# Kernel tuning notes

Measured on AMD Instinct MI355X. Metric: run time of the kernel, lower is better.

Reference implementation:

```python
import jax, jax.numpy as jnp
import numpy as np

N = 4096
F_IN = 256
HEADS = 8
FEAT = 64
NEG_SLOPE = 0.2


def setup_inputs() -> dict:
    key = jax.random.key(0)
    k_x, k_adj, k_w, k_s, k_d = jax.random.split(key, 5)
    x = jax.random.normal(k_x, (N, F_IN), dtype=jnp.float32)
    adj = (jax.random.uniform(k_adj, (N, N)) < 0.02).astype(jnp.float32)
    W = jax.random.normal(k_w, (F_IN, HEADS * FEAT), dtype=jnp.float32) * (1.0 / np.sqrt(F_IN))
    a_src = jax.random.normal(k_s, (FEAT,), dtype=jnp.float32) * (1.0 / np.sqrt(FEAT))
    a_dst = jax.random.normal(k_d, (FEAT,), dtype=jnp.float32) * (1.0 / np.sqrt(FEAT))
    return {"x": x, "adj": adj, "W": W, "a_src": a_src, "a_dst": a_dst}


def reference(x, adj, W, a_src, a_dst):
    n = x.shape[0]
    adj = adj + jnp.eye(n, dtype=adj.dtype)          # add self loops
    h = (x @ W).reshape(n, HEADS, FEAT)              # (N, H, F)
    s_src = jnp.einsum('nhf,f->nh', h, a_src)        # (N, H)
    s_dst = jnp.einsum('nhf,f->nh', h, a_dst)        # (N, H)
    # e[i, j, h] = leaky_relu(s_src[i,h] + s_dst[j,h])  -> (N, N, H)
    e = jax.nn.leaky_relu(s_src[:, None, :] + s_dst[None, :, :], negative_slope=NEG_SLOPE)
    mask = (adj == 0)                                # (N, N)
    e = jnp.where(mask[:, :, None], -1e9, e)
    alpha = jax.nn.softmax(e, axis=1)                # softmax over neighbor axis j
    out = jnp.einsum('ijh,jhf->ihf', alpha, h)       # (N, H, F)
    return out.reshape(n, HEADS * FEAT)              # concat heads -> (N, 512)
```

## Files before the change

### kernel.cpp

```cpp
#include <hip/hip_runtime.h>
#include <hip/hip_fp16.h>
#include <stdint.h>

#define NROWS 4096
#define FIN   256
#define NHEADS 8
#define HF    512
#define NEG   0.2f
#define MAXDEG 144

typedef _Float16 half8_t  __attribute__((ext_vector_type(8)));
typedef float    float4_t __attribute__((ext_vector_type(4)));

__global__ __launch_bounds__(256) void k_stage(const float* __restrict__ adj,
                                               const float* __restrict__ x,
                                               const float* __restrict__ W,
                                               uint16_t* __restrict__ nbr_g,
                                               int* __restrict__ deg,
                                               _Float16* __restrict__ xh,
                                               _Float16* __restrict__ Wt) {
    __shared__ uint16_t cnbr[4][MAXDEG];
    const int bid = blockIdx.x, t = threadIdx.x;

    if (bid < 1024) {
        const int w = t >> 6, lane = t & 63;
        const int row = bid*4 + w;

        uint32_t* nb32 = (uint32_t*)cnbr[w];
        nb32[lane] = 0;
        if (lane < (MAXDEG/2 - 64)) nb32[64 + lane] = 0;
        __builtin_amdgcn_wave_barrier();

        const float* ar = adj + (size_t)row * NROWS + lane*4;
        float4 f[16];
        #pragma unroll
        for (int k = 0; k < 16; ++k) f[k] = *(const float4*)(ar + k*256);

        uint64_t pm = 0;
        #pragma unroll
        for (int k = 0; k < 16; ++k) {
            if (f[k].x != 0.f) pm |= 1ull << (k*4+0);
            if (f[k].y != 0.f) pm |= 1ull << (k*4+1);
            if (f[k].z != 0.f) pm |= 1ull << (k*4+2);
            if (f[k].w != 0.f) pm |= 1ull << (k*4+3);
        }
        if (((row >> 2) & 63) == lane)
            pm |= 1ull << (((row >> 8) << 2) | (row & 3));

        int pcnt = __popcll(pm);
        int incl = pcnt;
        #pragma unroll
        for (int d = 1; d < 64; d <<= 1) {
            int u = __shfl_up(incl, d);
            if (lane >= d) incl += u;
        }
        int cnt = __shfl(incl, 63);
        int pos = incl - pcnt;
        if (cnt > MAXDEG) cnt = MAXDEG;

        uint64_t m = pm;
        while (m) {
            int q = (int)__ffsll((unsigned long long)m) - 1;  m &= m - 1;
            int col = ((q >> 2) << 8) + lane*4 + (q & 3);
            if (pos < MAXDEG) cnbr[w][pos] = (uint16_t)col;
            pos++;
        }
        __builtin_amdgcn_wave_barrier();

        uint32_t* og = (uint32_t*)(nbr_g + (size_t)row * MAXDEG);
        og[lane] = nb32[lane];
        if (lane < (MAXDEG/2 - 64)) og[64 + lane] = nb32[64 + lane];
        if (lane == 0) deg[row] = cnt;
    } else if (bid < 2048) {
        const int i4 = ((bid - 1024)*256 + t) * 4;
        float4 v = *(const float4*)&x[i4];
        union { _Float16 h[4]; uint2 u; } P;
        P.h[0] = (_Float16)v.x; P.h[1] = (_Float16)v.y;
        P.h[2] = (_Float16)v.z; P.h[3] = (_Float16)v.w;
        *(uint2*)&xh[i4] = P.u;
    } else {
        const int i4 = ((bid - 2048)*256 + t) * 4;
        const int n = i4 >> 8, k0 = i4 & 255;
        union { _Float16 h[4]; uint2 u; } P;
        P.h[0] = (_Float16)W[(size_t)(k0+0)*HF + n];
        P.h[1] = (_Float16)W[(size_t)(k0+1)*HF + n];
        P.h[2] = (_Float16)W[(size_t)(k0+2)*HF + n];
        P.h[3] = (_Float16)W[(size_t)(k0+3)*HF + n];
        *(uint2*)&Wt[(size_t)n*FIN + k0] = P.u;
    }
}

__global__ __launch_bounds__(256) void k_gemm(const _Float16* __restrict__ xh,
                                              const _Float16* __restrict__ Wt,
                                              const float* __restrict__ a_src,
                                              const float* __restrict__ a_dst,
                                              _Float16* __restrict__ hfp,
                                              float* __restrict__ s_src,
                                              float* __restrict__ s_dst) {
    __shared__ _Float16 Ah[64][72];
    __shared__ _Float16 Bh[64][72];
    const int t = threadIdx.x;
    const int bm = blockIdx.x >> 3, bn = blockIdx.x & 7;
    const int lane = t & 63, w = t >> 6;
    const int wm = (w & 1) * 32, wn = (w >> 1) * 32;
    const int mrow = lane & 15, kch = (lane >> 4) * 8;
    const int sr = t >> 2, sc = (t & 3) << 4;

    float4_t acc00{}, acc01{}, acc10{}, acc11{};

    for (int kt = 0; kt < FIN; kt += 64) {
        uint4 a0 = *(const uint4*)&xh[(size_t)(bm*64 + sr)*FIN + kt + sc];
        uint4 a1 = *(const uint4*)&xh[(size_t)(bm*64 + sr)*FIN + kt + sc + 8];
        uint4 b0 = *(const uint4*)&Wt[(size_t)(bn*64 + sr)*FIN + kt + sc];
        uint4 b1 = *(const uint4*)&Wt[(size_t)(bn*64 + sr)*FIN + kt + sc + 8];
        __syncthreads();
        *(uint4*)&Ah[sr][sc]     = a0;  *(uint4*)&Ah[sr][sc + 8] = a1;
        *(uint4*)&Bh[sr][sc]     = b0;  *(uint4*)&Bh[sr][sc + 8] = b1;
        __syncthreads();
        #pragma unroll
        for (int kk = 0; kk < 64; kk += 32) {
            half8_t fa0 = *(const half8_t*)&Ah[wm + mrow][kk + kch];
            half8_t fa1 = *(const half8_t*)&Ah[wm + 16 + mrow][kk + kch];
            half8_t fb0 = *(const half8_t*)&Bh[wn + mrow][kk + kch];
            half8_t fb1 = *(const half8_t*)&Bh[wn + 16 + mrow][kk + kch];
            acc00 = __builtin_amdgcn_mfma_f32_16x16x32_f16(fa0, fb0, acc00, 0, 0, 0);
            acc01 = __builtin_amdgcn_mfma_f32_16x16x32_f16(fa0, fb1, acc01, 0, 0, 0);
            acc10 = __builtin_amdgcn_mfma_f32_16x16x32_f16(fa1, fb0, acc10, 0, 0, 0);
            acc11 = __builtin_amdgcn_mfma_f32_16x16x32_f16(fa1, fb1, acc11, 0, 0, 0);
        }
    }

    __syncthreads();
    const int crow = (lane >> 4) * 4;
    #pragma unroll
    for (int r = 0; r < 4; ++r) {
        Ah[wm + crow + r][wn + mrow]           = (_Float16)acc00[r];
        Ah[wm + crow + r][wn + 16 + mrow]      = (_Float16)acc01[r];
        Ah[wm + 16 + crow + r][wn + mrow]      = (_Float16)acc10[r];
        Ah[wm + 16 + crow + r][wn + 16 + mrow] = (_Float16)acc11[r];
    }
    __syncthreads();

    uint4 h0 = *(const uint4*)&Ah[sr][sc];
    uint4 h1 = *(const uint4*)&Ah[sr][sc + 8];
    *(uint4*)&hfp[(size_t)(bm*64 + sr)*HF + bn*64 + sc]     = h0;
    *(uint4*)&hfp[(size_t)(bm*64 + sr)*HF + bn*64 + sc + 8] = h1;

    union { uint4 u[2]; _Float16 h[16]; } H; H.u[0] = h0; H.u[1] = h1;
    float ps = 0.f, pd = 0.f;
    #pragma unroll
    for (int e = 0; e < 16; ++e) {
        float hv = (float)H.h[e];
        ps += hv * a_src[sc + e];
        pd += hv * a_dst[sc + e];
    }
    ps += __shfl_xor(ps, 1); ps += __shfl_xor(ps, 2);
    pd += __shfl_xor(pd, 1); pd += __shfl_xor(pd, 2);
    if ((t & 3) == 0) {
        s_src[(bm*64 + sr)*NHEADS + bn] = ps;
        s_dst[(bm*64 + sr)*NHEADS + bn] = pd;
    }
}

__global__ __launch_bounds__(256) void k_agg(const uint16_t* __restrict__ nbr_g,
                                             const int* __restrict__ deg,
                                             const float* __restrict__ s_src,
                                             const float* __restrict__ s_dst,
                                             const _Float16* __restrict__ hfp,
                                             float* __restrict__ out) {
    __shared__ float    abuf[4][MAXDEG][8];
    __shared__ uint32_t nbrs[4][MAXDEG];
    __shared__ float    hsum[4][8];

    const int t = threadIdx.x, w = t >> 6, lane = t & 63;
    const int row = blockIdx.x * 4 + w;

    int cnt = deg[row];
    if (cnt > MAXDEG) cnt = MAXDEG;
    const int pad8 = (cnt + 7) & ~7;

    const uint32_t* src32 = (const uint32_t*)(nbr_g + (size_t)row * MAXDEG);
    uint32_t v0 = src32[lane];
    nbrs[w][2*lane]     = (v0 & 0xffffu) << 10;
    nbrs[w][2*lane + 1] = (v0 >> 16) << 10;
    if (lane < (MAXDEG/2 - 64)) {
        uint32_t v1 = src32[64 + lane];
        nbrs[w][128 + 2*lane] = (v1 & 0xffffu) << 10;
        nbrs[w][129 + 2*lane] = (v1 >> 16) << 10;
    }
    __builtin_amdgcn_wave_barrier();

    float4 si0 = *(const float4*)&s_src[row*NHEADS];
    float4 si1 = *(const float4*)&s_src[row*NHEADS + 4];
    float ac0=0,ac1=0,ac2=0,ac3=0,ac4=0,ac5=0,ac6=0,ac7=0;
    #pragma unroll 1
    for (int base = 0; base < pad8; base += 64) {
        int p = base + lane;
        if (p < pad8) {
            float a0=0,a1=0,a2=0,a3=0,a4=0,a5=0,a6=0,a7=0;
            if (p < cnt) {
                int j8 = (int)(nbrs[w][p] >> 10) * NHEADS;
                float4 d0 = *(const float4*)&s_dst[j8];
                float4 d1 = *(const float4*)&s_dst[j8 + 4];
                float e;
                e = si0.x + d0.x; e = e > 0.f ? e : NEG*e; a0 = __expf(e);
                e = si0.y + d0.y; e = e > 0.f ? e : NEG*e; a1 = __expf(e);
                e = si0.z + d0.z; e = e > 0.f ? e : NEG*e; a2 = __expf(e);
                e = si0.w + d0.w; e = e > 0.f ? e : NEG*e; a3 = __expf(e);
                e = si1.x + d1.x; e = e > 0.f ? e : NEG*e; a4 = __expf(e);
                e = si1.y + d1.y; e = e > 0.f ? e : NEG*e; a5 = __expf(e);
                e = si1.z + d1.z; e = e > 0.f ? e : NEG*e; a6 = __expf(e);
                e = si1.w + d1.w; e = e > 0.f ? e : NEG*e; a7 = __expf(e);
            }
            *(float4*)&abuf[w][p][0] = make_float4(a0, a1, a2, a3);
            *(float4*)&abuf[w][p][4] = make_float4(a4, a5, a6, a7);
            ac0+=a0; ac1+=a1; ac2+=a2; ac3+=a3; ac4+=a4; ac5+=a5; ac6+=a6; ac7+=a7;
        }
    }
    #pragma unroll
    for (int msk = 1; msk < 64; msk <<= 1) {
        ac0 += __shfl_xor(ac0, msk); ac1 += __shfl_xor(ac1, msk);
        ac2 += __shfl_xor(ac2, msk); ac3 += __shfl_xor(ac3, msk);
        ac4 += __shfl_xor(ac4, msk); ac5 += __shfl_xor(ac5, msk);
        ac6 += __shfl_xor(ac6, msk); ac7 += __shfl_xor(ac7, msk);
    }
    if (lane == 0) {
        hsum[w][0]=ac0; hsum[w][1]=ac1; hsum[w][2]=ac2; hsum[w][3]=ac3;
        hsum[w][4]=ac4; hsum[w][5]=ac5; hsum[w][6]=ac6; hsum[w][7]=ac7;
    }
    __builtin_amdgcn_wave_barrier();

    const int h3 = lane >> 3;
    const float invg = 1.f / hsum[w][h3];
    const uint32_t n0 = nbrs[w][lane];
    const uint32_t n1 = nbrs[w][64 + lane];
    const char* hbase = (const char*)hfp;
    float c0=0,c1=0,c2=0,c3=0,c4=0,c5=0,c6=0,c7=0;

#define GBATCH(JOEXPR)                                                      \
    {                                                                       \
        uint32_t jo[8]; uint4 hv[8]; float aa[8];                           \
        _Pragma("unroll") for (int u = 0; u < 8; ++u) jo[u] = (JOEXPR);     \
        _Pragma("unroll") for (int u = 0; u < 8; ++u)                       \
            hv[u] = *(const uint4*)(hbase + jo[u] + lane*16);               \
        _Pragma("unroll") for (int u = 0; u < 8; ++u)                       \
            aa[u] = abuf[w][p + u][h3];                                     \
        _Pragma("unroll") for (int u = 0; u < 8; ++u) {                     \
            union { uint4 q; _Float16 h[8]; } U; U.q = hv[u];               \
            c0 += (float)U.h[0]*aa[u]; c1 += (float)U.h[1]*aa[u];           \
            c2 += (float)U.h[2]*aa[u]; c3 += (float)U.h[3]*aa[u];           \
            c4 += (float)U.h[4]*aa[u]; c5 += (float)U.h[5]*aa[u];           \
            c6 += (float)U.h[6]*aa[u]; c7 += (float)U.h[7]*aa[u];           \
        }                                                                   \
    }

    const int e1 = pad8 < 64 ? pad8 : 64;
    for (int p = 0; p < e1; p += 8) GBATCH(__shfl(n0, p + u))
    if (pad8 > 64) {
        const int e2 = pad8 < 128 ? pad8 : 128;
        for (int p = 64; p < e2; p += 8) GBATCH(__shfl(n1, p + u - 64))
        for (int p = 128; p < pad8; p += 8) GBATCH(nbrs[w][p + u])
    }
#undef GBATCH

    float* orow = out + (size_t)row*HF + lane*8;
    *(float4*)(orow)     = make_float4(c0*invg, c1*invg, c2*invg, c3*invg);
    *(float4*)(orow + 4) = make_float4(c4*invg, c5*invg, c6*invg, c7*invg);
}

extern "C" void kernel_launch(void* const* d_in, const int* in_sizes, int n_in,
                              void* d_out, int out_size, void* d_ws, size_t ws_size,
                              hipStream_t stream) {
    const float* x     = (const float*)d_in[0];
    const float* adj   = (const float*)d_in[1];
    const float* W     = (const float*)d_in[2];
    const float* a_src = (const float*)d_in[3];
    const float* a_dst = (const float*)d_in[4];
    float* out = (float*)d_out;

    char* ws = (char*)d_ws;
    _Float16* hfp   = (_Float16*)ws;
    float*    s_src = (float*)(ws + 4u*1024*1024);
    float*    s_dst = (float*)(ws + 4u*1024*1024 + 128u*1024);
    _Float16* xh    = (_Float16*)(ws + 4u*1024*1024 + 256u*1024);
    _Float16* Wt    = (_Float16*)(ws + 6u*1024*1024 + 256u*1024);
    uint16_t* nbr_g = (uint16_t*)(ws + 6u*1024*1024 + 512u*1024);
    int*      deg   = (int*)(ws + 7u*1024*1024 + 768u*1024);

    k_stage<<<2176, 256, 0, stream>>>(adj, x, W, nbr_g, deg, xh, Wt);
    k_gemm <<<512,  256, 0, stream>>>(xh, Wt, a_src, a_dst, hfp, s_src, s_dst);
    k_agg  <<<1024, 256, 0, stream>>>(nbr_g, deg, s_src, s_dst, hfp, out);
}
```

Baseline: 47.88 us.

## Split aggregation across two waves per row and use nontemporal loads

```diff
diff --git a/kernel.cpp b/kernel.cpp
--- a/kernel.cpp
+++ b/kernel.cpp
@@ -11,6 +11,7 @@
 
 typedef _Float16 half8_t  __attribute__((ext_vector_type(8)));
 typedef float    float4_t __attribute__((ext_vector_type(4)));
+typedef float    f4v      __attribute__((ext_vector_type(4)));
 
 __global__ __launch_bounds__(256) void k_stage(const float* __restrict__ adj,
                                                const float* __restrict__ x,
@@ -31,10 +32,10 @@
         if (lane < (MAXDEG/2 - 64)) nb32[64 + lane] = 0;
         __builtin_amdgcn_wave_barrier();
 
-        const float* ar = adj + (size_t)row * NROWS + lane*4;
-        float4 f[16];
-        #pragma unroll
-        for (int k = 0; k < 16; ++k) f[k] = *(const float4*)(ar + k*256);
+        const f4v* ar = (const f4v*)(adj + (size_t)row * NROWS + lane*4);
+        f4v f[16];
+        #pragma unroll
+        for (int k = 0; k < 16; ++k) f[k] = __builtin_nontemporal_load(ar + k*64);
 
         uint64_t pm = 0;
         #pragma unroll
@@ -73,7 +74,7 @@
         if (lane == 0) deg[row] = cnt;
     } else if (bid < 2048) {
         const int i4 = ((bid - 1024)*256 + t) * 4;
-        float4 v = *(const float4*)&x[i4];
+        f4v v = __builtin_nontemporal_load((const f4v*)&x[i4]);
         union { _Float16 h[4]; uint2 u; } P;
         P.h[0] = (_Float16)v.x; P.h[1] = (_Float16)v.y;
         P.h[2] = (_Float16)v.z; P.h[3] = (_Float16)v.w;
@@ -162,18 +163,18 @@
     }
 }
 
-__global__ __launch_bounds__(256) void k_agg(const uint16_t* __restrict__ nbr_g,
-                                             const int* __restrict__ deg,
-                                             const float* __restrict__ s_src,
-                                             const float* __restrict__ s_dst,
-                                             const _Float16* __restrict__ hfp,
-                                             float* __restrict__ out) {
-    __shared__ float    abuf[4][MAXDEG][8];
-    __shared__ uint32_t nbrs[4][MAXDEG];
-    __shared__ float    hsum[4][8];
-
-    const int t = threadIdx.x, w = t >> 6, lane = t & 63;
-    const int row = blockIdx.x * 4 + w;
+__global__ __launch_bounds__(64) void k_agg(const uint16_t* __restrict__ nbr_g,
+                                            const int* __restrict__ deg,
+                                            const float* __restrict__ s_src,
+                                            const float* __restrict__ s_dst,
+                                            const _Float16* __restrict__ hfp,
+                                            float* __restrict__ out) {
+    __shared__ float    abuf[MAXDEG][4];
+    __shared__ uint32_t nbrs[MAXDEG];
+
+    const int lane = threadIdx.x;
+    const int wid  = blockIdx.x;
+    const int row  = wid >> 1, half = wid & 1;
 
     int cnt = deg[row];
     if (cnt > MAXDEG) cnt = MAXDEG;
@@ -181,91 +182,65 @@
 
     const uint32_t* src32 = (const uint32_t*)(nbr_g + (size_t)row * MAXDEG);
     uint32_t v0 = src32[lane];
-    nbrs[w][2*lane]     = (v0 & 0xffffu) << 10;
-    nbrs[w][2*lane + 1] = (v0 >> 16) << 10;
+    nbrs[2*lane]     = (v0 & 0xffffu) << 10;
+    nbrs[2*lane + 1] = (v0 >> 16) << 10;
     if (lane < (MAXDEG/2 - 64)) {
         uint32_t v1 = src32[64 + lane];
-        nbrs[w][128 + 2*lane] = (v1 & 0xffffu) << 10;
-        nbrs[w][129 + 2*lane] = (v1 >> 16) << 10;
+        nbrs[128 + 2*lane] = (v1 & 0xffffu) << 10;
+        nbrs[129 + 2*lane] = (v1 >> 16) << 10;
     }
     __builtin_amdgcn_wave_barrier();
 
-    float4 si0 = *(const float4*)&s_src[row*NHEADS];
-    float4 si1 = *(const float4*)&s_src[row*NHEADS + 4];
-    float ac0=0,ac1=0,ac2=0,ac3=0,ac4=0,ac5=0,ac6=0,ac7=0;
+    float4 si = *(const float4*)&s_src[row*NHEADS + half*4];
+    float ac0=0, ac1=0, ac2=0, ac3=0;
     #pragma unroll 1
     for (int base = 0; base < pad8; base += 64) {
         int p = base + lane;
         if (p < pad8) {
-            float a0=0,a1=0,a2=0,a3=0,a4=0,a5=0,a6=0,a7=0;
+            float a0=0, a1=0, a2=0, a3=0;
             if (p < cnt) {
-                int j8 = (int)(nbrs[w][p] >> 10) * NHEADS;
-                float4 d0 = *(const float4*)&s_dst[j8];
-                float4 d1 = *(const float4*)&s_dst[j8 + 4];
+                int j8 = (int)(nbrs[p] >> 10) * NHEADS;
+                float4 d = *(const float4*)&s_dst[j8 + half*4];
                 float e;
-                e = si0.x + d0.x; e = e > 0.f ? e : NEG*e; a0 = __expf(e);
-                e = si0.y + d0.y; e = e > 0.f ? e : NEG*e; a1 = __expf(e);
-                e = si0.z + d0.z; e = e > 0.f ? e : NEG*e; a2 = __expf(e);
-                e = si0.w + d0.w; e = e > 0.f ? e : NEG*e; a3 = __expf(e);
-                e = si1.x + d1.x; e = e > 0.f ? e : NEG*e; a4 = __expf(e);
-                e = si1.y + d1.y; e = e > 0.f ? e : NEG*e; a5 = __expf(e);
-                e = si1.z + d1.z; e = e > 0.f ? e : NEG*e; a6 = __expf(e);
-                e = si1.w + d1.w; e = e > 0.f ? e : NEG*e; a7 = __expf(e);
+                e = si.x + d.x; e = e > 0.f ? e : NEG*e; a0 = __expf(e);
+                e = si.y + d.y; e = e > 0.f ? e : NEG*e; a1 = __expf(e);
+                e = si.z + d.z; e = e > 0.f ? e : NEG*e; a2 = __expf(e);
+                e = si.w + d.w; e = e > 0.f ? e : NEG*e; a3 = __expf(e);
             }
-            *(float4*)&abuf[w][p][0] = make_float4(a0, a1, a2, a3);
-            *(float4*)&abuf[w][p][4] = make_float4(a4, a5, a6, a7);
-            ac0+=a0; ac1+=a1; ac2+=a2; ac3+=a3; ac4+=a4; ac5+=a5; ac6+=a6; ac7+=a7;
+            *(float4*)&abuf[p][0] = make_float4(a0, a1, a2, a3);
+            ac0 += a0; ac1 += a1; ac2 += a2; ac3 += a3;
         }
     }
     #pragma unroll
     for (int msk = 1; msk < 64; msk <<= 1) {
         ac0 += __shfl_xor(ac0, msk); ac1 += __shfl_xor(ac1, msk);
         ac2 += __shfl_xor(ac2, msk); ac3 += __shfl_xor(ac3, msk);
-        ac4 += __shfl_xor(ac4, msk); ac5 += __shfl_xor(ac5, msk);
-        ac6 += __shfl_xor(ac6, msk); ac7 += __shfl_xor(ac7, msk);
-    }
-    if (lane == 0) {
-        hsum[w][0]=ac0; hsum[w][1]=ac1; hsum[w][2]=ac2; hsum[w][3]=ac3;
-        hsum[w][4]=ac4; hsum[w][5]=ac5; hsum[w][6]=ac6; hsum[w][7]=ac7;
-    }
+    }
+    const int h3 = lane >> 4;
+    float tot = (h3 == 0) ? ac0 : (h3 == 1) ? ac1 : (h3 == 2) ? ac2 : ac3;
+    const float invg = 1.f / tot;
     __builtin_amdgcn_wave_barrier();
 
-    const int h3 = lane >> 3;
-    const float invg = 1.f / hsum[w][h3];
-    const uint32_t n0 = nbrs[w][lane];
-    const uint32_t n1 = nbrs[w][64 + lane];
-    const char* hbase = (const char*)hfp;
-    float c0=0,c1=0,c2=0,c3=0,c4=0,c5=0,c6=0,c7=0;
-
-#define GBATCH(JOEXPR)                                                      \
-    {                                                                       \
-        uint32_t jo[8]; uint4 hv[8]; float aa[8];                           \
-        _Pragma("unroll") for (int u = 0; u < 8; ++u) jo[u] = (JOEXPR);     \
-        _Pragma("unroll") for (int u = 0; u < 8; ++u)                       \
-            hv[u] = *(const uint4*)(hbase + jo[u] + lane*16);               \
-        _Pragma("unroll") for (int u = 0; u < 8; ++u)                       \
-            aa[u] = abuf[w][p + u][h3];                                     \
-        _Pragma("unroll") for (int u = 0; u < 8; ++u) {                     \
-            union { uint4 q; _Float16 h[8]; } U; U.q = hv[u];               \
-            c0 += (float)U.h[0]*aa[u]; c1 += (float)U.h[1]*aa[u];           \
-            c2 += (float)U.h[2]*aa[u]; c3 += (float)U.h[3]*aa[u];           \
-            c4 += (float)U.h[4]*aa[u]; c5 += (float)U.h[5]*aa[u];           \
-            c6 += (float)U.h[6]*aa[u]; c7 += (float)U.h[7]*aa[u];           \
-        }                                                                   \
-    }
-
-    const int e1 = pad8 < 64 ? pad8 : 64;
-    for (int p = 0; p < e1; p += 8) GBATCH(__shfl(n0, p + u))
-    if (pad8 > 64) {
-        const int e2 = pad8 < 128 ? pad8 : 128;
-        for (int p = 64; p < e2; p += 8) GBATCH(__shfl(n1, p + u - 64))
-        for (int p = 128; p < pad8; p += 8) GBATCH(nbrs[w][p + u])
-    }
-#undef GBATCH
-
-    float* orow = out + (size_t)row*HF + lane*8;
-    *(float4*)(orow)     = make_float4(c0*invg, c1*invg, c2*invg, c3*invg);
-    *(float4*)(orow + 4) = make_float4(c4*invg, c5*invg, c6*invg, c7*invg);
+    const char* hb = (const char*)hfp + half*512 + lane*8;
+    float c0=0, c1=0, c2=0, c3=0;
+    for (int p = 0; p < pad8; p += 8) {
+        uint32_t jo[8]; uint2 hv[8]; float aa[8];
+        #pragma unroll
+        for (int u = 0; u < 8; ++u) jo[u] = nbrs[p + u];
+        #pragma unroll
+        for (int u = 0; u < 8; ++u) hv[u] = *(const uint2*)(hb + jo[u]);
+        #pragma unroll
+        for (int u = 0; u < 8; ++u) aa[u] = abuf[p + u][h3];
+        #pragma unroll
+        for (int u = 0; u < 8; ++u) {
+            union { uint2 q; _Float16 h[4]; } U; U.q = hv[u];
+            c0 += (float)U.h[0]*aa[u]; c1 += (float)U.h[1]*aa[u];
+            c2 += (float)U.h[2]*aa[u]; c3 += (float)U.h[3]*aa[u];
+        }
+    }
+
+    f4v o; o.x = c0*invg; o.y = c1*invg; o.z = c2*invg; o.w = c3*invg;
+    __builtin_nontemporal_store(o, (f4v*)&out[(size_t)row*HF + half*256 + lane*4]);
 }
 
 extern "C" void kernel_launch(void* const* d_in, const int* in_sizes, int n_in,
@@ -289,5 +264,5 @@
 
     k_stage<<<2176, 256, 0, stream>>>(adj, x, W, nbr_g, deg, xh, Wt);
     k_gemm <<<512,  256, 0, stream>>>(xh, Wt, a_src, a_dst, hfp, s_src, s_dst);
-    k_agg  <<<1024, 256, 0, stream>>>(nbr_g, deg, s_src, s_dst, hfp, out);
-}
+    k_agg  <<<8192, 64,  0, stream>>>(nbr_g, deg, s_src, s_dst, hfp, out);
+}
```

Result: slower. 55.19 us (+15.3%).
